# Optimization experiments

Hardware: AMD Instinct MI355X
Metric: run time of the kernel (lower is better)

Reference implementation:

```python
import jax, jax.numpy as jnp
import numpy as np

B, N, D = 32, 1024, 128


def setup_inputs() -> dict:
    key = jax.random.key(0)
    ks = jax.random.split(key, 8)
    scale = 0.05
    P = jax.random.normal(ks[0], (B, N, D), dtype=jnp.float32)
    w_itr_att = jax.random.normal(ks[1], (3 * D,), dtype=jnp.float32) * scale
    w1 = jax.random.normal(ks[2], (2 * D, D), dtype=jnp.float32) * scale
    w2 = jax.random.normal(ks[3], (2 * D, D), dtype=jnp.float32) * scale
    w3 = jax.random.normal(ks[4], (2 * D, D), dtype=jnp.float32) * scale
    b1 = jnp.zeros((D,), dtype=jnp.float32)
    b2 = jnp.zeros((D,), dtype=jnp.float32)
    b3 = jnp.zeros((D,), dtype=jnp.float32)
    return {"P": P, "w_itr_att": w_itr_att, "w1": w1, "w2": w2,
            "w3": w3, "b1": b1, "b2": b2, "b3": b3}


def reference(P, w_itr_att, w1, w2, w3, b1, b2, b3):
    # P: [b, n, d]
    d = P.shape[-1]
    # Original builds alphaP[b,i,:,j] = concat(P[b,j], P[b,i], P[b,j]*P[b,i])
    # and A[b,i,j] = w_itr_att . alphaP[b,i,:,j]. Decompose w to avoid the
    # O(n^2 * 3d) tensor while computing identical math.
    wa, wb, wc = w_itr_att[:d], w_itr_att[d:2 * d], w_itr_att[2 * d:]
    A = (P @ wb)[:, :, None] + (P @ wa)[:, None, :] \
        + jnp.einsum('bid,bjd->bij', P * wc, P)  # [b, n, n]
    SA = jax.nn.softmax(A, axis=-1)              # softmax over j (axis=2)
    itr_attn = jnp.einsum('bij,bjd->bid', SA, P)  # batch_dot(SA, P)
    # Fuse gate (dropout is identity at inference)
    P_concat = jnp.concatenate([P, itr_attn], axis=2)  # [b, n, 2d]
    z = jnp.tanh(P_concat @ w1 + b1)
    r = jax.nn.sigmoid(P_concat @ w2 + b2)
    f = jax.nn.sigmoid(P_concat @ w3 + b3)
    return r * P + f * z
```

## Files before the change

kernel.cpp:

```cpp
#include <hip/hip_runtime.h>
#include <math.h>

#define BB 32
#define NN 1024
#define DD 128

typedef __bf16 bf16;
typedef bf16 bf16x4 __attribute__((ext_vector_type(4)));
typedef bf16 bf16x8 __attribute__((ext_vector_type(8)));
typedef float f32x4 __attribute__((ext_vector_type(4)));
typedef float f32x16 __attribute__((ext_vector_type(16)));

#define MFMA16(a, b, c) __builtin_amdgcn_mfma_f32_16x16x32_bf16(a, b, c, 0, 0, 0)
#define MFMA32(a, b, c) __builtin_amdgcn_mfma_f32_32x32x16_bf16(a, b, c, 0, 0, 0)

__device__ inline bf16x4 swap32(bf16x4 v) {
    union { bf16x4 h; int i[2]; } u, r;
    u.h = v;
    r.i[0] = __shfl_xor(u.i[0], 32, 64);
    r.i[1] = __shfl_xor(u.i[1], 32, 64);
    return r.h;
}

#define LTS 133
__global__ __launch_bounds__(256) void k_prep(const float* __restrict__ P,
                                              const float* __restrict__ w_itr,
                                              bf16* __restrict__ Xbf,
                                              bf16* __restrict__ Pq,
                                              bf16* __restrict__ Ptp,
                                              float* __restrict__ t) {
    __shared__ float Lt[64 * LTS];
    int tid = threadIdx.x;
    int b = blockIdx.x >> 4, g = blockIdx.x & 15;
    int n0 = g * 64;
    long base = ((long)b * NN + n0) * DD;
#pragma unroll
    for (int i = 0; i < 8; ++i) {
        int idx = tid + i * 256;
        int row = idx >> 5, c4 = idx & 31;
        *(float4*)&Lt[row * LTS + c4 * 4] = *(const float4*)&P[base + row * 128 + c4 * 4];
    }
    __syncthreads();
    {
        int row = tid >> 2, q = tid & 3;
        float s = 0.f;
#pragma unroll
        for (int kk = 0; kk < 32; ++kk) {
            int k = 4 * kk + q;
            s += Lt[row * LTS + k] * w_itr[k];
        }
        s += __shfl_xor(s, 1);
        s += __shfl_xor(s, 2);
        if (q == 0) t[(long)b * NN + n0 + row] = s;
    }
    const float* wc = w_itr + 2 * DD;
#pragma unroll
    for (int i = 0; i < 4; ++i) {
        int idx = tid + i * 256;
        int row = idx >> 4, seg = idx & 15;
        float4 va = *(const float4*)&Lt[row * LTS + seg * 8];
        float4 vb = *(const float4*)&Lt[row * LTS + seg * 8 + 4];
        float4 wa4 = *(const float4*)&wc[seg * 8];
        float4 wb4 = *(const float4*)&wc[seg * 8 + 4];
        float fv[8] = {va.x, va.y, va.z, va.w, vb.x, vb.y, vb.z, vb.w};
        float wv[8] = {wa4.x, wa4.y, wa4.z, wa4.w, wb4.x, wb4.y, wb4.z, wb4.w};
        bf16x8 xv, qv;
#pragma unroll
        for (int e = 0; e < 8; ++e) {
            xv[e] = (bf16)fv[e];
            qv[e] = (bf16)(fv[e] * wv[e]);
        }
        long rowg = (long)b * NN + n0 + row;
        *(bf16x8*)&Xbf[rowg * 128 + seg * 8] = xv;
        *(bf16x8*)&Pq[rowg * 128 + seg * 8] = qv;
    }
#pragma unroll
    for (int i = 0; i < 4; ++i) {
        int idx = tid + i * 256;
        int d = idx >> 3, c = idx & 7;
        bf16x8 v;
#pragma unroll
        for (int e = 0; e < 8; ++e) v[e] = (bf16)Lt[(c * 8 + e) * LTS + d];
        *(bf16x8*)&Ptp[((long)b * DD + d) * NN + n0 + c * 8] = v;
    }
}

__global__ __launch_bounds__(256) void k_prepw(const float* __restrict__ w1,
                                               const float* __restrict__ w2,
                                               const float* __restrict__ w3,
                                               bf16* __restrict__ WtG) {
    __shared__ float Lw[32][33];
    int bi = blockIdx.x;
    int mat = bi >> 5, rem = bi & 31;
    int kt = rem >> 2, ct = rem & 3;
    const float* wsrc = (mat == 0) ? w1 : ((mat == 1) ? w2 : w3);
    int tid = threadIdx.x;
#pragma unroll
    for (int p = 0; p < 4; ++p) {
        int idx = tid + p * 256;
        int kr = idx >> 5, c = idx & 31;
        Lw[kr][c] = wsrc[(kt * 32 + kr) * DD + ct * 32 + c];
    }
    __syncthreads();
    int colg = tid >> 3, kq = tid & 7;
    bf16x4 v;
#pragma unroll
    for (int e = 0; e < 4; ++e) v[e] = (bf16)Lw[kq * 4 + e][colg];
    *(bf16x4*)&WtG[(mat * 128 + ct * 32 + colg) * 256 + kt * 32 + kq * 4] = v;
}

__global__ __launch_bounds__(256, 3) void k_attn(const bf16* __restrict__ Xbf,
                                                 const bf16* __restrict__ Pq,
                                                 const bf16* __restrict__ Ptp,
                                                 const float* __restrict__ t,
                                                 const bf16* __restrict__ WtG,
                                                 const float* __restrict__ b1,
                                                 const float* __restrict__ b2,
                                                 const float* __restrict__ b3,
                                                 float* __restrict__ out) {
    __shared__ __align__(16) char smem[52736];
    bf16* Kt = (bf16*)smem;
    bf16* Vt = (bf16*)(smem + 17408);
    float* tsh = (float*)(smem + 35840);
    float* lbuf = (float*)(smem + 52224);
    bf16* Xsh = (bf16*)smem;
    bf16* Obf = (bf16*)(smem + 33792);
    bf16* Wst = (bf16*)(smem + 33792);

    const int tid = threadIdx.x;
    const int w = tid >> 6, lane = tid & 63;
    const int col = lane & 31, q = lane >> 5;
    const int kh = w >> 1, rg = w & 1;
    const int b = blockIdx.x & 31, qt = blockIdx.x >> 5;
    const long qrow0 = (long)b * NN + qt * 64;
    const long qbase = qrow0 + rg * 32;

    bf16x8 Qb[8];
#pragma unroll
    for (int c = 0; c < 8; ++c)
        Qb[c] = *(const bf16x8*)&Pq[(qbase + col) * 128 + c * 16 + q * 8];

    f32x16 O[4];
#pragma unroll
    for (int mt = 0; mt < 4; ++mt)
#pragma unroll
        for (int r = 0; r < 16; ++r) O[mt][r] = 0.f;
    float lsum = 0.f;

    float4 kr[4], vr[4];
    float tr = 0.f;
    auto loadKV = [&](int jt) {
        int j0 = jt * 64;
#pragma unroll
        for (int i = 0; i < 4; ++i) {
            int idx = tid + i * 256;
            kr[i] = *(const float4*)&Xbf[((long)b * NN + j0 + (idx >> 4)) * 128 +
                                         (idx & 15) * 8];
            vr[i] = *(const float4*)&Ptp[((long)b * DD + (idx >> 3)) * NN + j0 +
                                         (idx & 7) * 8];
        }
        tr = (tid < 64) ? t[(long)b * NN + j0 + tid] : 0.f;
    };

    loadKV(0);
    for (int jt = 0; jt < 16; ++jt) {
        __syncthreads();
#pragma unroll
        for (int i = 0; i < 4; ++i) {
            int idx = tid + i * 256;
            *(float4*)&Kt[(idx >> 4) * 136 + (idx & 15) * 8] = kr[i];
            *(float4*)&Vt[(idx >> 3) * 72 + (idx & 7) * 8] = vr[i];
        }
        if (tid < 64) tsh[tid] = tr;
        __syncthreads();
        if (jt < 15) loadKV(jt + 1);

        const bf16* KtH = Kt + kh * 32 * 136;
        const float* tH = tsh + kh * 32;

        f32x16 S;
#pragma unroll
        for (int r = 0; r < 16; ++r) S[r] = 0.f;
#pragma unroll
        for (int c = 0; c < 8; ++c)
            S = MFMA32(*(const bf16x8*)&KtH[col * 136 + c * 16 + q * 8], Qb[c], S);
        float tqs[16];
#pragma unroll
        for (int i = 0; i < 4; ++i) {
            float4 tv = *(const float4*)&tH[8 * i + 4 * q];
            tqs[4 * i + 0] = tv.x; tqs[4 * i + 1] = tv.y;
            tqs[4 * i + 2] = tv.z; tqs[4 * i + 3] = tv.w;
        }
        float pv[16];
#pragma unroll
        for (int r = 0; r < 16; ++r) {
            float e = __expf(fminf(S[r] + tqs[r], 80.f));
            pv[r] = e;
            lsum += e;
        }
        bf16x4 Qd[4];
#pragma unroll
        for (int i = 0; i < 4; ++i)
#pragma unroll
            for (int e = 0; e < 4; ++e) Qd[i][e] = (bf16)pv[4 * i + e];
        bf16x4 sA = q ? Qd[0] : Qd[1];
        bf16x4 rA = swap32(sA);
        bf16x4 sB = q ? Qd[2] : Qd[3];
        bf16x4 rB = swap32(sB);
        bf16x4 lo0 = q ? rA : Qd[0], hi0 = q ? Qd[1] : rA;
        bf16x4 lo1 = q ? rB : Qd[2], hi1 = q ? Qd[3] : rB;
        bf16x8 f0, f1;
#pragma unroll
        for (int e = 0; e < 4; ++e) {
            f0[e] = lo0[e]; f0[4 + e] = hi0[e];
            f1[e] = lo1[e]; f1[4 + e] = hi1[e];
        }
#pragma unroll
        for (int mt = 0; mt < 4; ++mt) {
            O[mt] = MFMA32(*(const bf16x8*)&Vt[(mt * 32 + col) * 72 + kh * 32 + q * 8],
                           f0, O[mt]);
            O[mt] = MFMA32(*(const bf16x8*)&Vt[(mt * 32 + col) * 72 + kh * 32 + 16 + q * 8],
                           f1, O[mt]);
        }
    }

    float l2 = lsum + __shfl_xor(lsum, 32, 64);
    if (q == 0) lbuf[(kh * 2 + rg) * 32 + col] = l2;
    __syncthreads();
    if (kh == 1) {
#pragma unroll
        for (int mt = 0; mt < 4; ++mt)
#pragma unroll
            for (int r = 0; r < 16; ++r) {
                int d = mt * 32 + (r & 3) + 8 * (r >> 2) + 4 * q;
                Obf[(rg * 128 + d) * 36 + col] = (bf16)O[mt][r];
            }
    } else {
#pragma unroll
        for (int i = 0; i < 8; ++i) {
            int idx = tid + i * 128;
            int row = idx >> 4, seg = idx & 15;
            *(bf16x8*)&Xsh[row * 264 + seg * 8] =
                *(const bf16x8*)&Xbf[(qrow0 + row) * 128 + seg * 8];
        }
    }
    __syncthreads();
    if (kh == 0) {
        float linv = 1.f / (lbuf[rg * 32 + col] + lbuf[(2 + rg) * 32 + col]);
#pragma unroll
        for (int mt = 0; mt < 4; ++mt)
#pragma unroll
            for (int r = 0; r < 16; ++r) {
                int d = mt * 32 + (r & 3) + 8 * (r >> 2) + 4 * q;
                float v = (O[mt][r] + (float)Obf[(rg * 128 + d) * 36 + col]) * linv;
                Xsh[(rg * 32 + col) * 264 + 128 + d] = (bf16)v;
            }
    }

    const int ln = lane & 15, q3 = lane >> 4;
    f32x4 gz[8], gr[8];
#pragma unroll
    for (int mat = 0; mat < 3; ++mat) {
        f32x4 acc[8];
#pragma unroll
        for (int nt = 0; nt < 8; ++nt) acc[nt] = (f32x4){0.f, 0.f, 0.f, 0.f};
#pragma unroll
        for (int k2 = 0; k2 < 4; ++k2) {
            __syncthreads();
#pragma unroll
            for (int i = 0; i < 4; ++i) {
                int idx = tid + i * 256;
                *(float4*)&Wst[(idx >> 3) * 72 + (idx & 7) * 8] =
                    *(const float4*)&WtG[(mat * 128 + (idx >> 3)) * 256 + k2 * 64 +
                                         (idx & 7) * 8];
            }
            __syncthreads();
#pragma unroll
            for (int kc2 = 0; kc2 < 2; ++kc2) {
                bf16x8 Af = *(const bf16x8*)&Xsh[(w * 16 + ln) * 264 + k2 * 64 +
                                                 kc2 * 32 + q3 * 8];
#pragma unroll
                for (int nt = 0; nt < 8; ++nt) {
                    bf16x8 Bf = *(const bf16x8*)&Wst[(nt * 16 + ln) * 72 + kc2 * 32 + q3 * 8];
                    acc[nt] = MFMA16(Af, Bf, acc[nt]);
                }
            }
        }
        const float* bp = (mat == 0) ? b1 : ((mat == 1) ? b2 : b3);
#pragma unroll
        for (int nt = 0; nt < 8; ++nt) {
            int colc = nt * 16 + ln;
            float bb = bp[colc];
#pragma unroll
            for (int r = 0; r < 4; ++r) {
                float y = acc[nt][r] + bb;
                if (mat == 0) gz[nt][r] = tanhf(y);
                else if (mat == 1) gr[nt][r] = 1.f / (1.f + __expf(-y));
                else {
                    float fg = 1.f / (1.f + __expf(-y));
                    int lrow = w * 16 + q3 * 4 + r;
                    float p = (float)Xsh[lrow * 264 + colc];
                    out[(qrow0 + lrow) * 128 + colc] = gr[nt][r] * p + fg * gz[nt][r];
                }
            }
        }
    }
}

extern "C" void kernel_launch(void* const* d_in, const int* in_sizes, int n_in,
                              void* d_out, int out_size, void* d_ws, size_t ws_size,
                              hipStream_t stream) {
    const float* P     = (const float*)d_in[0];
    const float* w_itr = (const float*)d_in[1];
    const float* w1    = (const float*)d_in[2];
    const float* w2    = (const float*)d_in[3];
    const float* w3    = (const float*)d_in[4];
    const float* b1    = (const float*)d_in[5];
    const float* b2    = (const float*)d_in[6];
    const float* b3    = (const float*)d_in[7];
    float* out = (float*)d_out;

    char* wsb = (char*)d_ws;
    bf16* Xbf  = (bf16*)(wsb);
    bf16* Pq   = (bf16*)(wsb + 8388608);
    bf16* Ptp  = (bf16*)(wsb + 16777216);
    float* tws = (float*)(wsb + 25165824);
    bf16* WtG  = (bf16*)(wsb + 25296896);

    k_prep<<<dim3(BB * 16), dim3(256), 0, stream>>>(P, w_itr, Xbf, Pq, Ptp, tws);
    k_prepw<<<dim3(96), dim3(256), 0, stream>>>(w1, w2, w3, WtG);
    k_attn<<<dim3(512), dim3(256), 0, stream>>>(Xbf, Pq, Ptp, tws, WtG, b1, b2, b3, out);
}
```

Baseline: 200.6 us.

## Split KV range across four waves per 32-row query tile, drop LDS staging

Each block now handles 32 query rows instead of 64, and its four waves each process a disjoint quarter of the key range. Every wave loads K and V fragments straight from global memory into registers, with no LDS staging and no block barriers inside the loop. Partial outputs and row sums are combined through shared memory in a two-step reduction. The grid doubles, and the gate GEMM output goes through LDS so global stores are coalesced. The cost is redundant K/V global reads across blocks, extra reduction traffic, and no explicit prefetch of the next tile.

```diff
diff --git a/kernel.cpp b/kernel.cpp
--- a/kernel.cpp
+++ b/kernel.cpp
@@ -118,27 +118,24 @@
                                                  const float* __restrict__ b2,
                                                  const float* __restrict__ b3,
                                                  float* __restrict__ out) {
-    __shared__ __align__(16) char smem[52736];
-    bf16* Kt = (bf16*)smem;
-    bf16* Vt = (bf16*)(smem + 17408);
-    float* tsh = (float*)(smem + 35840);
-    float* lbuf = (float*)(smem + 52224);
-    bf16* Xsh = (bf16*)smem;
-    bf16* Obf = (bf16*)(smem + 33792);
-    bf16* Wst = (bf16*)(smem + 33792);
+    __shared__ __align__(16) char smem[51200];
+    float* PA   = (float*)smem;
+    bf16*  Wst  = (bf16*)smem;
+    float* ost  = (float*)smem;
+    bf16*  Xsh  = (bf16*)(smem + 33792);
+    float* lbuf = (float*)(smem + 50688);
 
     const int tid = threadIdx.x;
-    const int w = tid >> 6, lane = tid & 63;
+    const int kh = tid >> 6, lane = tid & 63;
     const int col = lane & 31, q = lane >> 5;
-    const int kh = w >> 1, rg = w & 1;
     const int b = blockIdx.x & 31, qt = blockIdx.x >> 5;
-    const long qrow0 = (long)b * NN + qt * 64;
-    const long qbase = qrow0 + rg * 32;
+    const long qrow0 = (long)b * NN + qt * 32;
+    const long kvrow = (long)b * NN;
 
     bf16x8 Qb[8];
 #pragma unroll
     for (int c = 0; c < 8; ++c)
-        Qb[c] = *(const bf16x8*)&Pq[(qbase + col) * 128 + c * 16 + q * 8];
+        Qb[c] = *(const bf16x8*)&Pq[(qrow0 + col) * 128 + c * 16 + q * 8];
 
     f32x16 O[4];
 #pragma unroll
@@ -147,50 +144,32 @@
         for (int r = 0; r < 16; ++r) O[mt][r] = 0.f;
     float lsum = 0.f;
 
-    float4 kr[4], vr[4];
-    float tr = 0.f;
-    auto loadKV = [&](int jt) {
-        int j0 = jt * 64;
+    for (int kt = 0; kt < 8; ++kt) {
+        int j0 = kh * 256 + kt * 32;
+        bf16x8 kf[8];
+#pragma unroll
+        for (int c = 0; c < 8; ++c)
+            kf[c] = *(const bf16x8*)&Xbf[(kvrow + j0 + col) * 128 + c * 16 + q * 8];
+        bf16x8 vf[4][2];
+#pragma unroll
+        for (int mt = 0; mt < 4; ++mt)
+#pragma unroll
+            for (int kc = 0; kc < 2; ++kc)
+                vf[mt][kc] = *(const bf16x8*)&Ptp[((long)b * DD + mt * 32 + col) * NN +
+                                                  j0 + kc * 16 + q * 8];
+        float tqs[16];
 #pragma unroll
         for (int i = 0; i < 4; ++i) {
-            int idx = tid + i * 256;
-            kr[i] = *(const float4*)&Xbf[((long)b * NN + j0 + (idx >> 4)) * 128 +
-                                         (idx & 15) * 8];
-            vr[i] = *(const float4*)&Ptp[((long)b * DD + (idx >> 3)) * NN + j0 +
-                                         (idx & 7) * 8];
-        }
-        tr = (tid < 64) ? t[(long)b * NN + j0 + tid] : 0.f;
-    };
-
-    loadKV(0);
-    for (int jt = 0; jt < 16; ++jt) {
-        __syncthreads();
-#pragma unroll
-        for (int i = 0; i < 4; ++i) {
-            int idx = tid + i * 256;
-            *(float4*)&Kt[(idx >> 4) * 136 + (idx & 15) * 8] = kr[i];
-            *(float4*)&Vt[(idx >> 3) * 72 + (idx & 7) * 8] = vr[i];
-        }
-        if (tid < 64) tsh[tid] = tr;
-        __syncthreads();
-        if (jt < 15) loadKV(jt + 1);
-
-        const bf16* KtH = Kt + kh * 32 * 136;
-        const float* tH = tsh + kh * 32;
-
-        f32x16 S;
-#pragma unroll
-        for (int r = 0; r < 16; ++r) S[r] = 0.f;
-#pragma unroll
-        for (int c = 0; c < 8; ++c)
-            S = MFMA32(*(const bf16x8*)&KtH[col * 136 + c * 16 + q * 8], Qb[c], S);
-        float tqs[16];
-#pragma unroll
-        for (int i = 0; i < 4; ++i) {
-            float4 tv = *(const float4*)&tH[8 * i + 4 * q];
+            float4 tv = *(const float4*)&t[kvrow + j0 + 8 * i + 4 * q];
             tqs[4 * i + 0] = tv.x; tqs[4 * i + 1] = tv.y;
             tqs[4 * i + 2] = tv.z; tqs[4 * i + 3] = tv.w;
         }
+        f32x16 S;
+#pragma unroll
+        for (int r = 0; r < 16; ++r) S[r] = 0.f;
+#pragma unroll
+        for (int c = 0; c < 8; ++c) S = MFMA32(kf[c], Qb[c], S);
+
         float pv[16];
 #pragma unroll
         for (int r = 0; r < 16; ++r) {
@@ -217,28 +196,48 @@
         }
 #pragma unroll
         for (int mt = 0; mt < 4; ++mt) {
-            O[mt] = MFMA32(*(const bf16x8*)&Vt[(mt * 32 + col) * 72 + kh * 32 + q * 8],
-                           f0, O[mt]);
-            O[mt] = MFMA32(*(const bf16x8*)&Vt[(mt * 32 + col) * 72 + kh * 32 + 16 + q * 8],
-                           f1, O[mt]);
+            O[mt] = MFMA32(vf[mt][0], f0, O[mt]);
+            O[mt] = MFMA32(vf[mt][1], f1, O[mt]);
         }
     }
 
     float l2 = lsum + __shfl_xor(lsum, 32, 64);
-    if (q == 0) lbuf[(kh * 2 + rg) * 32 + col] = l2;
-    __syncthreads();
-    if (kh == 1) {
+    if (q == 0) lbuf[kh * 32 + col] = l2;
+    if (kh & 1) {
+        int slot = kh >> 1;
 #pragma unroll
         for (int mt = 0; mt < 4; ++mt)
 #pragma unroll
             for (int r = 0; r < 16; ++r) {
                 int d = mt * 32 + (r & 3) + 8 * (r >> 2) + 4 * q;
-                Obf[(rg * 128 + d) * 36 + col] = (bf16)O[mt][r];
-            }
-    } else {
-#pragma unroll
-        for (int i = 0; i < 8; ++i) {
-            int idx = tid + i * 128;
+                PA[slot * 4224 + d * 33 + col] = O[mt][r];
+            }
+    }
+    __syncthreads();
+    if (!(kh & 1)) {
+        int slot = kh >> 1;
+#pragma unroll
+        for (int mt = 0; mt < 4; ++mt)
+#pragma unroll
+            for (int r = 0; r < 16; ++r) {
+                int d = mt * 32 + (r & 3) + 8 * (r >> 2) + 4 * q;
+                O[mt][r] += PA[slot * 4224 + d * 33 + col];
+            }
+    }
+    __syncthreads();
+    if (kh == 2) {
+#pragma unroll
+        for (int mt = 0; mt < 4; ++mt)
+#pragma unroll
+            for (int r = 0; r < 16; ++r) {
+                int d = mt * 32 + (r & 3) + 8 * (r >> 2) + 4 * q;
+                PA[d * 33 + col] = O[mt][r];
+            }
+    } else if (kh & 1) {
+        int t128 = (kh >> 1) * 64 + lane;
+#pragma unroll
+        for (int i = 0; i < 4; ++i) {
+            int idx = t128 + i * 128;
             int row = idx >> 4, seg = idx & 15;
             *(bf16x8*)&Xsh[row * 264 + seg * 8] =
                 *(const bf16x8*)&Xbf[(qrow0 + row) * 128 + seg * 8];
@@ -246,24 +245,27 @@
     }
     __syncthreads();
     if (kh == 0) {
-        float linv = 1.f / (lbuf[rg * 32 + col] + lbuf[(2 + rg) * 32 + col]);
+        float ltot = lbuf[col] + lbuf[32 + col] + lbuf[64 + col] + lbuf[96 + col];
+        float linv = 1.f / ltot;
 #pragma unroll
         for (int mt = 0; mt < 4; ++mt)
 #pragma unroll
             for (int r = 0; r < 16; ++r) {
                 int d = mt * 32 + (r & 3) + 8 * (r >> 2) + 4 * q;
-                float v = (O[mt][r] + (float)Obf[(rg * 128 + d) * 36 + col]) * linv;
-                Xsh[(rg * 32 + col) * 264 + 128 + d] = (bf16)v;
+                float v = (O[mt][r] + PA[d * 33 + col]) * linv;
+                Xsh[col * 264 + 128 + d] = (bf16)v;
             }
     }
 
     const int ln = lane & 15, q3 = lane >> 4;
-    f32x4 gz[8], gr[8];
+    const int rh = kh & 1, ch = kh >> 1;
+    f32x4 gz[4], gr[4];
+    float rres[16];
 #pragma unroll
     for (int mat = 0; mat < 3; ++mat) {
-        f32x4 acc[8];
-#pragma unroll
-        for (int nt = 0; nt < 8; ++nt) acc[nt] = (f32x4){0.f, 0.f, 0.f, 0.f};
+        f32x4 acc[4];
+#pragma unroll
+        for (int nt = 0; nt < 4; ++nt) acc[nt] = (f32x4){0.f, 0.f, 0.f, 0.f};
 #pragma unroll
         for (int k2 = 0; k2 < 4; ++k2) {
             __syncthreads();
@@ -277,19 +279,20 @@
             __syncthreads();
 #pragma unroll
             for (int kc2 = 0; kc2 < 2; ++kc2) {
-                bf16x8 Af = *(const bf16x8*)&Xsh[(w * 16 + ln) * 264 + k2 * 64 +
+                bf16x8 Af = *(const bf16x8*)&Xsh[(rh * 16 + ln) * 264 + k2 * 64 +
                                                  kc2 * 32 + q3 * 8];
 #pragma unroll
-                for (int nt = 0; nt < 8; ++nt) {
-                    bf16x8 Bf = *(const bf16x8*)&Wst[(nt * 16 + ln) * 72 + kc2 * 32 + q3 * 8];
+                for (int nt = 0; nt < 4; ++nt) {
+                    bf16x8 Bf = *(const bf16x8*)&Wst[(ch * 64 + nt * 16 + ln) * 72 +
+                                                     kc2 * 32 + q3 * 8];
                     acc[nt] = MFMA16(Af, Bf, acc[nt]);
                 }
             }
         }
         const float* bp = (mat == 0) ? b1 : ((mat == 1) ? b2 : b3);
 #pragma unroll
-        for (int nt = 0; nt < 8; ++nt) {
-            int colc = nt * 16 + ln;
+        for (int nt = 0; nt < 4; ++nt) {
+            int colc = ch * 64 + nt * 16 + ln;
             float bb = bp[colc];
 #pragma unroll
             for (int r = 0; r < 4; ++r) {
@@ -298,12 +301,26 @@
                 else if (mat == 1) gr[nt][r] = 1.f / (1.f + __expf(-y));
                 else {
                     float fg = 1.f / (1.f + __expf(-y));
-                    int lrow = w * 16 + q3 * 4 + r;
+                    int lrow = rh * 16 + q3 * 4 + r;
                     float p = (float)Xsh[lrow * 264 + colc];
-                    out[(qrow0 + lrow) * 128 + colc] = gr[nt][r] * p + fg * gz[nt][r];
+                    rres[nt * 4 + r] = gr[nt][r] * p + fg * gz[nt][r];
                 }
             }
         }
+    }
+    __syncthreads();
+#pragma unroll
+    for (int nt = 0; nt < 4; ++nt)
+#pragma unroll
+        for (int r = 0; r < 4; ++r)
+            ost[(rh * 16 + q3 * 4 + r) * 132 + ch * 64 + nt * 16 + ln] = rres[nt * 4 + r];
+    __syncthreads();
+#pragma unroll
+    for (int i = 0; i < 4; ++i) {
+        int idx = tid + i * 256;
+        int row = idx >> 5, c4 = idx & 31;
+        float4 v = *(const float4*)&ost[row * 132 + c4 * 4];
+        *(float4*)&out[(qrow0 + row) * 128 + c4 * 4] = v;
     }
 }
 
@@ -329,5 +346,5 @@
 
     k_prep<<<dim3(BB * 16), dim3(256), 0, stream>>>(P, w_itr, Xbf, Pq, Ptp, tws);
     k_prepw<<<dim3(96), dim3(256), 0, stream>>>(w1, w2, w3, WtG);
-    k_attn<<<dim3(512), dim3(256), 0, stream>>>(Xbf, Pq, Ptp, tws, WtG, b1, b2, b3, out);
-}
+    k_attn<<<dim3(1024), dim3(256), 0, stream>>>(Xbf, Pq, Ptp, tws, WtG, b1, b2, b3, out);
+}
```

After: 176.6 us. 1.14x faster.
